# Optimization experiments

Measured on AMD Instinct MI355X. Metric: run time of the kernel, lower is better.

## Reference

```python
import jax, jax.numpy as jnp
import numpy as np

B, C_IN, T = 32, 22, 5000
EMB, P = 64, 100
HOP, NFFT, SR = 25, 128, 250
MIN_SZ, MAX_SZ = 10, 100
OC = 40
SCALES = (9, 25, 49)
FC = OC * len(SCALES)
_freqs = np.arange(NFFT // 2 + 1) * SR / NFFT
MU_IDX = np.nonzero((_freqs >= 8) & (_freqs <= 13))[0]   # bins 5,6
BETA_IDX = np.nonzero((_freqs >= 13) & (_freqs <= 30))[0]  # bins 7..15


def setup_inputs() -> dict:
    key = jax.random.key(0)
    k = iter(jax.random.split(key, 16))
    inp = {"x": jax.random.normal(next(k), (B, C_IN, T), jnp.float32)}
    for i, s in enumerate(SCALES):
        inp[f"ms{i}_w1"] = jax.random.normal(next(k), (OC, 1, 1, s), jnp.float32) * 0.05
        inp[f"ms{i}_b1"] = jnp.zeros((OC,), jnp.float32)
        inp[f"ms{i}_w2"] = jax.random.normal(next(k), (OC, OC, C_IN, 1), jnp.float32) * 0.05
        inp[f"ms{i}_b2"] = jnp.zeros((OC,), jnp.float32)
        inp[f"ms{i}_g"] = jnp.ones((OC,), jnp.float32)
        inp[f"ms{i}_bt"] = jnp.zeros((OC,), jnp.float32)
        inp[f"ms{i}_m"] = jnp.zeros((OC,), jnp.float32)
        inp[f"ms{i}_v"] = jnp.ones((OC,), jnp.float32)
    inp["a_w1"] = jax.random.normal(next(k), (C_IN // 2, C_IN, 3), jnp.float32) * 0.05
    inp["a_b1"] = jnp.zeros((C_IN // 2,), jnp.float32)
    inp["a_g"] = jnp.ones((C_IN // 2,), jnp.float32)
    inp["a_bt"] = jnp.zeros((C_IN // 2,), jnp.float32)
    inp["a_m"] = jnp.zeros((C_IN // 2,), jnp.float32)
    inp["a_v"] = jnp.ones((C_IN // 2,), jnp.float32)
    inp["a_w2"] = jax.random.normal(next(k), (1, C_IN // 2, 1), jnp.float32) * 0.05
    inp["a_b2"] = jnp.zeros((1,), jnp.float32)
    inp["proj_w"] = jax.random.normal(next(k), (EMB, FC, 1), jnp.float32) * 0.05
    inp["proj_b"] = jnp.zeros((EMB,), jnp.float32)
    return inp


def _conv1d(x, w, pad):
    return jax.lax.conv_general_dilated(x, w, (1,), [(pad, pad)],
                                        dimension_numbers=("NCH", "OIH", "NCH"))


def _bn(y, g, bt, m, v):  # eval-mode BatchNorm over channel dim of [B, C, T]
    return (y - m[None, :, None]) * jax.lax.rsqrt(v[None, :, None] + 1e-5) * g[None, :, None] + bt[None, :, None]


def _branch(x, w1, b1, w2, b2, g, bt, m, v):
    # Conv2d(1,OC,(1,ks)) on [B,1,C,T] == per-channel 1D conv over time.
    oc, _, _, ks = w1.shape
    b_, c_, t_ = x.shape
    y = _conv1d(x.reshape(b_ * c_, 1, t_), w1.reshape(oc, 1, ks), (ks - 1) // 2) + b1[None, :, None]
    y = y.reshape(b_, c_, oc, t_).transpose(0, 2, 1, 3)            # [B, OC, C, T]
    # Conv2d(OC,OC,(C,1)) collapses the channel (height) dim.
    y = jnp.einsum("oih,biht->bot", w2[..., 0], y) + b2[None, :, None]
    return jax.nn.elu(_bn(y, g, bt, m, v))                         # [B, OC, T]


def _stft_power(x):
    # torchaudio Spectrogram: center=True, reflect pad, periodic hann, power=2
    pad = NFFT // 2
    xp = jnp.pad(x, ((0, 0), (0, 0), (pad, pad)), mode="reflect")
    nfr = T // HOP  # module truncates to t // hop frames
    idx = jnp.arange(nfr)[:, None] * HOP + jnp.arange(NFFT)[None, :]
    win = 0.5 * (1.0 - jnp.cos(2.0 * jnp.pi * jnp.arange(NFFT) / NFFT))
    frames = xp[..., idx] * win                                    # [B, C, nfr, NFFT]
    spec = jnp.fft.rfft(frames, axis=-1)
    return spec.real ** 2 + spec.imag ** 2                         # [B, C, nfr, NFFT//2+1]


def _interp_linear(a, n):  # F.interpolate(mode='linear', align_corners=False) on [B, L]
    L = a.shape[-1]
    pos = jnp.clip((jnp.arange(n) + 0.5) * (L / n) - 0.5, 0.0, L - 1.0)
    lo = jnp.floor(pos).astype(jnp.int32)
    hi = jnp.minimum(lo + 1, L - 1)
    w = pos - lo
    return a[:, lo] * (1.0 - w) + a[:, hi] * w


def _adaptive_grid(act):
    w = 1.0 / (act + 1e-6)
    w = w / jnp.sum(w, axis=1, keepdims=True)
    gs = jnp.clip(w * T, MIN_SZ, MAX_SZ)
    gs = gs * (T / jnp.sum(gs, axis=1, keepdims=True))
    gsr = jnp.round(gs).astype(jnp.int32)
    gsr = gsr.at[:, -1].add(T - jnp.sum(gsr, axis=1))
    gsf = jnp.clip(gsr, MIN_SZ, MAX_SZ)
    gsf = gsf.at[:, -1].add(T - jnp.sum(gsf, axis=1))
    return jnp.where(gsf < MIN_SZ, MIN_SZ, gsf)


def _forward(x, ms0_w1, ms0_b1, ms0_w2, ms0_b2, ms0_g, ms0_bt, ms0_m, ms0_v,
             ms1_w1, ms1_b1, ms1_w2, ms1_b2, ms1_g, ms1_bt, ms1_m, ms1_v,
             ms2_w1, ms2_b1, ms2_w2, ms2_b2, ms2_g, ms2_bt, ms2_m, ms2_v,
             a_w1, a_b1, a_g, a_bt, a_m, a_v, a_w2, a_b2, proj_w, proj_b):
    # ---- frequency-domain activity detector ----
    spec = _stft_power(x)                                          # [B, C, 200, F]
    comb = spec[..., MU_IDX].mean(-1) + spec[..., BETA_IDX].mean(-1)  # [B, C, 200]
    a = jax.nn.relu(_bn(_conv1d(comb, a_w1, 1) + a_b1[None, :, None], a_g, a_bt, a_m, a_v))
    a = jnp.einsum("oi,bit->bot", a_w2[..., 0], a)[:, 0] + a_b2[0]
    activity = jax.nn.sigmoid(a)                                   # [B, 200]
    act_i = _interp_linear(activity, P)                            # [B, P]
    grid = _adaptive_grid(act_i)                                   # [B, P] int32, sums ~= T
    ends = jnp.cumsum(grid, axis=1)
    starts = ends - grid
    # ---- multi-scale CNN features ----
    feats = jnp.concatenate([
        _branch(x, ms0_w1, ms0_b1, ms0_w2, ms0_b2, ms0_g, ms0_bt, ms0_m, ms0_v),
        _branch(x, ms1_w1, ms1_b1, ms1_w2, ms1_b2, ms1_g, ms1_bt, ms1_m, ms1_v),
        _branch(x, ms2_w1, ms2_b1, ms2_w2, ms2_b2, ms2_g, ms2_bt, ms2_m, ms2_v)],
        axis=1)                                                    # [B, FC, T]
    # ---- ragged per-patch avg+max pooling via segment reductions ----
    tix = jnp.arange(T)
    seg = jax.vmap(lambda e: jnp.searchsorted(e, tix, side="right"))(ends)  # [B,T] in [0,P]
    flat = (seg + jnp.arange(B)[:, None] * (P + 1)).reshape(-1)
    f = feats.transpose(0, 2, 1).reshape(B * T, FC)
    nseg = B * (P + 1)  # extra slot collects any overflow timesteps
    sums = jax.ops.segment_sum(f, flat, num_segments=nseg)
    cnt = jax.ops.segment_sum(jnp.ones((B * T, 1), f.dtype), flat, num_segments=nseg)
    mx = jax.ops.segment_max(f, flat, num_segments=nseg)
    avg = sums / jnp.maximum(cnt, 1.0)
    mx = jnp.where(cnt > 0, mx, 0.0)
    pooled = (avg + mx).reshape(B, P + 1, FC)[:, :P]               # combined avg+max
    valid = ((ends <= T) & (starts < ends))[..., None]
    pooled = jnp.where(valid, pooled, 0.0)
    emb = jnp.einsum("oc,bpc->bpo", proj_w[..., 0], pooled) + proj_b  # [B, P, EMB]
    return emb, grid, act_i


def reference(x, ms0_w1, ms0_b1, ms0_w2, ms0_b2, ms0_g, ms0_bt, ms0_m, ms0_v,
              ms1_w1, ms1_b1, ms1_w2, ms1_b2, ms1_g, ms1_bt, ms1_m, ms1_v,
              ms2_w1, ms2_b1, ms2_w2, ms2_b2, ms2_g, ms2_bt, ms2_m, ms2_v,
              a_w1, a_b1, a_g, a_bt, a_m, a_v, a_w2, a_b2, proj_w, proj_b):
    return _forward(x, ms0_w1, ms0_b1, ms0_w2, ms0_b2, ms0_g, ms0_bt, ms0_m, ms0_v,
                    ms1_w1, ms1_b1, ms1_w2, ms1_b2, ms1_g, ms1_bt, ms1_m, ms1_v,
                    ms2_w1, ms2_b1, ms2_w2, ms2_b2, ms2_g, ms2_bt, ms2_m, ms2_v,
                    a_w1, a_b1, a_g, a_bt, a_m, a_v, a_w2, a_b2, proj_w, proj_b)
```

## Files before the change

### kernel.cpp

```cpp
#include <hip/hip_runtime.h>
#include <hip/hip_bf16.h>
#include <hip/hip_fp8.h>
#include <math.h>
#include <string.h>

#define B 32
#define CIN 22
#define T 5000
#define EMB 64
#define P 100
#define HOP 25
#define OC 40
#define FC 120
#define NBIN 11
#define NFR 200

#define TCH 256
#define CROWS 304
#define RS8 40

#define XPAD 5128
#define TWROW 24

#define PLANE ((size_t)B * T * OC)

typedef __attribute__((ext_vector_type(4))) float f32x4;

__device__ __forceinline__ unsigned short f2bf(float f) {
  unsigned u = __float_as_uint(f);
  unsigned r = (u + 0x7FFFu + ((u >> 16) & 1u)) >> 16;
  return (unsigned short)r;
}
__device__ __forceinline__ float bf2f(unsigned short u) {
  return __uint_as_float(((unsigned)u) << 16);
}
__device__ __forceinline__ unsigned char f2fp8(float f) {
  __hip_fp8_e4m3 q(f);
  return (unsigned char)q.__x;
}
__device__ __forceinline__ float fast_elu(float y) {
  return y > 0.f ? y : (__builtin_amdgcn_exp2f(y * 1.44269504088896340736f) - 1.0f);
}
__device__ __forceinline__ unsigned pack2bf(float a, float b) {
  __hip_bfloat162 h = __float22bfloat162_rn(make_float2(a, b));
  unsigned u;
  memcpy(&u, &h, 4);
  return u;
}
__device__ __forceinline__ float wave_sum_f(float v) {
  #pragma unroll
  for (int off = 1; off < 64; off <<= 1) v += __shfl_xor(v, off);
  return v;
}
__device__ __forceinline__ int wave_sum_i(int v) {
  #pragma unroll
  for (int off = 1; off < 64; off <<= 1) v += __shfl_xor(v, off);
  return v;
}

struct SetupArgs {
  const float* w1[3]; const float* b1[3]; const float* w2[3]; const float* b2[3];
  const float* g[3];  const float* bt[3]; const float* m[3];  const float* v[3];
  unsigned char* pw8;
  float* A; float* Bc; float* tw;
};

__global__ __launch_bounds__(256) void setup_all(SetupArgs args) {
  int bx = blockIdx.x;
  int tid = threadIdx.x;
  if (bx < 63) {
    int id = bx * 256 + tid;
    if (id < 15936) {
      int fi = id >> 6;
      int lane = id & 63;
      int s, KS, fl;
      if (fi < 27)       { s = 0; KS = 9;  fl = fi; }
      else if (fi < 102) { s = 1; KS = 25; fl = fi - 27; }
      else               { s = 2; KS = 49; fl = fi - 102; }
      int k = fl / 3, ot = fl - k * 3;
      int m = lane & 15, hb = (lane >> 4) << 3;
      int o = ot * 16 + m;
      float val[8];
      #pragma unroll
      for (int j = 0; j < 8; ++j) val[j] = 0.f;
      if (o < OC && hb < CIN) {
        const float* w1 = args.w1[s];
        const float* w2 = args.w2[s];
        if (hb + 8 <= CIN) {
          for (int i = 0; i < OC; ++i) {
            float wv = w1[i * KS + k];
            const float* w2r = w2 + (size_t)(o * OC + i) * CIN + hb;
            float2 a0 = *(const float2*)(w2r + 0);
            float2 a1 = *(const float2*)(w2r + 2);
            float2 a2 = *(const float2*)(w2r + 4);
            float2 a3 = *(const float2*)(w2r + 6);
            val[0] = fmaf(a0.x, wv, val[0]); val[1] = fmaf(a0.y, wv, val[1]);
            val[2] = fmaf(a1.x, wv, val[2]); val[3] = fmaf(a1.y, wv, val[3]);
            val[4] = fmaf(a2.x, wv, val[4]); val[5] = fmaf(a2.y, wv, val[5]);
            val[6] = fmaf(a3.x, wv, val[6]); val[7] = fmaf(a3.y, wv, val[7]);
          }
        } else {
          for (int i = 0; i < OC; ++i) {
            float wv = w1[i * KS + k];
            const float* w2r = w2 + (size_t)(o * OC + i) * CIN + hb;
            float2 a0 = *(const float2*)(w2r + 0);
            float2 a1 = *(const float2*)(w2r + 2);
            float2 a2 = *(const float2*)(w2r + 4);
            val[0] = fmaf(a0.x, wv, val[0]); val[1] = fmaf(a0.y, wv, val[1]);
            val[2] = fmaf(a1.x, wv, val[2]); val[3] = fmaf(a1.y, wv, val[3]);
            val[4] = fmaf(a2.x, wv, val[4]); val[5] = fmaf(a2.y, wv, val[5]);
          }
        }
      }
      unsigned char bytes[8];
      #pragma unroll
      for (int j = 0; j < 8; ++j) bytes[j] = f2fp8(val[j]);
      long long pk;
      memcpy(&pk, bytes, 8);
      *(long long*)(args.pw8 + (size_t)fi * 512 + lane * 8) = pk;
    }
  } else if (bx < 69) {
    int id = (bx - 63) * 256 + tid;
    if (id < 1408) {
      int n = id & 127, k = id >> 7;
      const double PI = 3.14159265358979323846;
      double ang = -2.0 * PI * (double)((k + 5) * n) / 128.0;
      double win = 0.5 * (1.0 - cos(2.0 * PI * (double)n / 128.0));
      args.tw[n * TWROW + 2 * k]     = (float)(cos(ang) * win);
      args.tw[n * TWROW + 2 * k + 1] = (float)(sin(ang) * win);
    } else if (id < 1536) {
      int n = id - 1408;
      args.tw[n * TWROW + 22] = 0.f;
      args.tw[n * TWROW + 23] = 0.f;
    }
  } else {
    if (tid < 120) {
      int s = tid / 40, o = tid - s * 40;
      const float* w2 = args.w2[s];
      float sc = args.g[s][o] / sqrtf(args.v[s][o] + 1e-5f);
      float cc = args.b2[s][o];
      for (int i = 0; i < OC; ++i) {
        float sh = 0.f;
        for (int h = 0; h < CIN; ++h) sh += w2[(o * OC + i) * CIN + h];
        cc = fmaf(args.b1[s][i], sh, cc);
      }
      args.A[tid] = sc;
      args.Bc[tid] = cc * sc + (args.bt[s][o] - args.m[s][o] * sc);
    }
  }
}

__global__ __launch_bounds__(256) void stft_comb(const float* __restrict__ x,
                                                 const float* __restrict__ tw,
                                                 float* __restrict__ comb) {
  __shared__ float xsh[XPAD];
  int bc = blockIdx.x;
  const float* xr = x + (size_t)bc * T;
  int tid = threadIdx.x;
  for (int i = tid; i < XPAD; i += 256) {
    int mm = i - 64;
    mm = (mm < 0) ? -mm : mm;
    mm = (mm >= T) ? (2 * T - 2 - mm) : mm;
    xsh[i] = xr[mm];
  }
  __syncthreads();
  int fr = tid;
  if (fr < NFR) {
    float cr[NBIN], ci[NBIN];
    #pragma unroll
    for (int k = 0; k < NBIN; ++k) { cr[k] = 0.f; ci[k] = 0.f; }
    const float* xw = xsh + fr * HOP;
    #pragma unroll 2
    for (int n = 0; n < 128; ++n) {
      float xv = xw[n];
      const float4* t4 = reinterpret_cast<const float4*>(tw + n * TWROW);
      float4 w0 = t4[0], w1 = t4[1], w2 = t4[2], w3 = t4[3], w4 = t4[4], w5 = t4[5];
      cr[0] = fmaf(xv, w0.x, cr[0]); ci[0] = fmaf(xv, w0.y, ci[0]);
      cr[1] = fmaf(xv, w0.z, cr[1]); ci[1] = fmaf(xv, w0.w, ci[1]);
      cr[2] = fmaf(xv, w1.x, cr[2]); ci[2] = fmaf(xv, w1.y, ci[2]);
      cr[3] = fmaf(xv, w1.z, cr[3]); ci[3] = fmaf(xv, w1.w, ci[3]);
      cr[4] = fmaf(xv, w2.x, cr[4]); ci[4] = fmaf(xv, w2.y, ci[4]);
      cr[5] = fmaf(xv, w2.z, cr[5]); ci[5] = fmaf(xv, w2.w, ci[5]);
      cr[6] = fmaf(xv, w3.x, cr[6]); ci[6] = fmaf(xv, w3.y, ci[6]);
      cr[7] = fmaf(xv, w3.z, cr[7]); ci[7] = fmaf(xv, w3.w, ci[7]);
      cr[8] = fmaf(xv, w4.x, cr[8]); ci[8] = fmaf(xv, w4.y, ci[8]);
      cr[9] = fmaf(xv, w4.z, cr[9]); ci[9] = fmaf(xv, w4.w, ci[9]);
      cr[10] = fmaf(xv, w5.x, cr[10]); ci[10] = fmaf(xv, w5.y, ci[10]);
    }
    float p[NBIN];
    #pragma unroll
    for (int k = 0; k < NBIN; ++k) p[k] = cr[k] * cr[k] + ci[k] * ci[k];
    float beta = 0.f;
    #pragma unroll
    for (int k = 2; k < NBIN; ++k) beta += p[k];
    comb[bc * NFR + fr] = 0.5f * (p[0] + p[1]) + beta * (1.f / 9.f);
  }
}

struct MidSmem {
  union {
    struct {
      float cl[CIN * NFR];
      float actL[NFR];
      float aiL[P];
      float fL[P];
      int giL[P];
      int sI[P];
      float red;
    } a;
    unsigned char xs8[CROWS * RS8];
  };
};

template <int KS, int FB, int SBASE>
__device__ __forceinline__ void scale_body(const unsigned char* __restrict__ xs8,
                                           const unsigned char* __restrict__ pw8,
                                           const float* __restrict__ Aff,
                                           const float* __restrict__ Bff,
                                           unsigned short* __restrict__ fplane,
                                           int b, int t0, int wt0, int lane) {
  constexpr int PAD = (KS - 1) / 2;
  const int n = lane & 15, q = lane >> 4;
  f32x4 acc[3][4];
  #pragma unroll
  for (int ot = 0; ot < 3; ++ot)
    #pragma unroll
    for (int ti = 0; ti < 4; ++ti)
      acc[ot][ti] = (f32x4){0.f, 0.f, 0.f, 0.f};

  const unsigned char* pws = pw8 + (size_t)FB * 512 + lane * 8;
  const unsigned char* xrow = xs8 + (24 - PAD + wt0 + n) * RS8 + q * 8;
  long long A0 = *(const long long*)(pws);
  long long A1 = *(const long long*)(pws + 512);
  long long A2 = *(const long long*)(pws + 1024);
  long long B0 = *(const long long*)(xrow);
  long long B1 = *(const long long*)(xrow + 16 * RS8);
  long long B2 = *(const long long*)(xrow + 32 * RS8);
  long long B3 = *(const long long*)(xrow + 48 * RS8);
  #pragma unroll 2
  for (int k = 0; k < KS - 1; ++k) {
    const unsigned char* p = pws + (size_t)(k + 1) * 1536;
    long long nA0 = *(const long long*)(p);
    long long nA1 = *(const long long*)(p + 512);
    long long nA2 = *(const long long*)(p + 1024);
    const unsigned char* xr = xrow + (k + 1) * RS8;
    long long nB0 = *(const long long*)(xr);
    long long nB1 = *(const long long*)(xr + 16 * RS8);
    long long nB2 = *(const long long*)(xr + 32 * RS8);
    long long nB3 = *(const long long*)(xr + 48 * RS8);
    acc[0][0] = __builtin_amdgcn_mfma_f32_16x16x32_fp8_fp8(A0, B0, acc[0][0], 0, 0, 0);
    acc[1][0] = __builtin_amdgcn_mfma_f32_16x16x32_fp8_fp8(A1, B0, acc[1][0], 0, 0, 0);
    acc[2][0] = __builtin_amdgcn_mfma_f32_16x16x32_fp8_fp8(A2, B0, acc[2][0], 0, 0, 0);
    acc[0][1] = __builtin_amdgcn_mfma_f32_16x16x32_fp8_fp8(A0, B1, acc[0][1], 0, 0, 0);
    acc[1][1] = __builtin_amdgcn_mfma_f32_16x16x32_fp8_fp8(A1, B1, acc[1][1], 0, 0, 0);
    acc[2][1] = __builtin_amdgcn_mfma_f32_16x16x32_fp8_fp8(A2, B1, acc[2][1], 0, 0, 0);
    acc[0][2] = __builtin_amdgcn_mfma_f32_16x16x32_fp8_fp8(A0, B2, acc[0][2], 0, 0, 0);
    acc[1][2] = __builtin_amdgcn_mfma_f32_16x16x32_fp8_fp8(A1, B2, acc[1][2], 0, 0, 0);
    acc[2][2] = __builtin_amdgcn_mfma_f32_16x16x32_fp8_fp8(A2, B2, acc[2][2], 0, 0, 0);
    acc[0][3] = __builtin_amdgcn_mfma_f32_16x16x32_fp8_fp8(A0, B3, acc[0][3], 0, 0, 0);
    acc[1][3] = __builtin_amdgcn_mfma_f32_16x16x32_fp8_fp8(A1, B3, acc[1][3], 0, 0, 0);
    acc[2][3] = __builtin_amdgcn_mfma_f32_16x16x32_fp8_fp8(A2, B3, acc[2][3], 0, 0, 0);
    A0 = nA0; A1 = nA1; A2 = nA2;
    B0 = nB0; B1 = nB1; B2 = nB2; B3 = nB3;
  }
  acc[0][0] = __builtin_amdgcn_mfma_f32_16x16x32_fp8_fp8(A0, B0, acc[0][0], 0, 0, 0);
  acc[1][0] = __builtin_amdgcn_mfma_f32_16x16x32_fp8_fp8(A1, B0, acc[1][0], 0, 0, 0);
  acc[2][0] = __builtin_amdgcn_mfma_f32_16x16x32_fp8_fp8(A2, B0, acc[2][0], 0, 0, 0);
  acc[0][1] = __builtin_amdgcn_mfma_f32_16x16x32_fp8_fp8(A0, B1, acc[0][1], 0, 0, 0);
  acc[1][1] = __builtin_amdgcn_mfma_f32_16x16x32_fp8_fp8(A1, B1, acc[1][1], 0, 0, 0);
  acc[2][1] = __builtin_amdgcn_mfma_f32_16x16x32_fp8_fp8(A2, B1, acc[2][1], 0, 0, 0);
  acc[0][2] = __builtin_amdgcn_mfma_f32_16x16x32_fp8_fp8(A0, B2, acc[0][2], 0, 0, 0);
  acc[1][2] = __builtin_amdgcn_mfma_f32_16x16x32_fp8_fp8(A1, B2, acc[1][2], 0, 0, 0);
  acc[2][2] = __builtin_amdgcn_mfma_f32_16x16x32_fp8_fp8(A2, B2, acc[2][2], 0, 0, 0);
  acc[0][3] = __builtin_amdgcn_mfma_f32_16x16x32_fp8_fp8(A0, B3, acc[0][3], 0, 0, 0);
  acc[1][3] = __builtin_amdgcn_mfma_f32_16x16x32_fp8_fp8(A1, B3, acc[1][3], 0, 0, 0);
  acc[2][3] = __builtin_amdgcn_mfma_f32_16x16x32_fp8_fp8(A2, B3, acc[2][3], 0, 0, 0);

  #pragma unroll
  for (int ot = 0; ot < 3; ++ot) {
    int obase = ot * 16 + q * 4;
    if (obase < OC) {
      float Av0 = Aff[SBASE + obase + 0], Bv0 = Bff[SBASE + obase + 0];
      float Av1 = Aff[SBASE + obase + 1], Bv1 = Bff[SBASE + obase + 1];
      float Av2 = Aff[SBASE + obase + 2], Bv2 = Bff[SBASE + obase + 2];
      float Av3 = Aff[SBASE + obase + 3], Bv3 = Bff[SBASE + obase + 3];
      #pragma unroll
      for (int ti = 0; ti < 4; ++ti) {
        int tt = t0 + wt0 + ti * 16 + n;
        if (tt < T) {
          uint2 pk;
          pk.x = pack2bf(fast_elu(fmaf(acc[ot][ti][0], Av0, Bv0)),
                         fast_elu(fmaf(acc[ot][ti][1], Av1, Bv1)));
          pk.y = pack2bf(fast_elu(fmaf(acc[ot][ti][2], Av2, Bv2)),
                         fast_elu(fmaf(acc[ot][ti][3], Av3, Bv3)));
          *reinterpret_cast<uint2*>(fplane + (size_t)(b * T + tt) * OC + obase) = pk;
        }
      }
    }
  }
}

struct MidArgs {
  const float* x;
  const unsigned char* pw8;
  const float* Aff; const float* Bff;
  unsigned short* feats;
  const float* comb;
  const float* aw1; const float* ab1;
  const float* ag;  const float* abt;
  const float* am;  const float* av;
  const float* aw2; const float* ab2;
  float* out_grid; float* out_acti;
  int* ends_i; int* grid_i;
};

__global__ __launch_bounds__(256) void mid_all(MidArgs args) {
  __shared__ MidSmem sm;
  int bx = blockIdx.x;
  int tid = threadIdx.x;
  if (bx >= B) {
    int cx = bx - B;
    int b = cx / 20, t0 = (cx - b * 20) * TCH;
    for (int i = tid; i < CROWS * RS8 / 4; i += 256)
      reinterpret_cast<unsigned*>(sm.xs8)[i] = 0u;
    __syncthreads();
    for (int idx = tid; idx < CIN * CROWS; idx += 256) {
      int h = idx / CROWS, tl = idx - h * CROWS;
      int gt = t0 - 24 + tl;
      float v = (gt >= 0 && gt < T) ? args.x[(size_t)(b * CIN + h) * T + gt] : 0.f;
      sm.xs8[tl * RS8 + h] = f2fp8(v);
    }
    __syncthreads();
    int wv = tid >> 6, lane = tid & 63;
    int wt0 = wv * 64;
    scale_body<9, 0, 0>(sm.xs8, args.pw8, args.Aff, args.Bff, args.feats, b, t0, wt0, lane);
    scale_body<25, 27, 40>(sm.xs8, args.pw8, args.Aff, args.Bff, args.feats + PLANE, b, t0, wt0, lane);
    scale_body<49, 102, 80>(sm.xs8, args.pw8, args.Aff, args.Bff, args.feats + 2 * PLANE, b, t0, wt0, lane);
  } else {
    int b = bx;
    for (int i = tid; i < CIN * NFR; i += 256) sm.a.cl[i] = args.comb[b * CIN * NFR + i];
    __syncthreads();
    int t = tid;
    if (t < NFR) {
      float z = args.ab2[0];
      for (int o = 0; o < 11; ++o) {
        float s = args.ab1[o];
        for (int i = 0; i < CIN; ++i) {
          const float* wr = args.aw1 + o * 66 + i * 3;
          const float* crow = sm.a.cl + i * NFR;
          if (t > 0)       s = fmaf(wr[0], crow[t - 1], s);
          s = fmaf(wr[1], crow[t], s);
          if (t < NFR - 1) s = fmaf(wr[2], crow[t + 1], s);
        }
        float rs = 1.0f / sqrtf(args.av[o] + 1e-5f);
        float y = (s - args.am[o]) * rs * args.ag[o] + args.abt[o];
        y = fmaxf(y, 0.f);
        z = fmaf(args.aw2[o], y, z);
      }
      sm.a.actL[t] = 1.f / (1.f + expf(-z));
    }
    __syncthreads();
    if (t < P) {
      float ai = 0.5f * (sm.a.actL[2 * t] + sm.a.actL[2 * t + 1]);
      sm.a.aiL[t] = ai;
      args.out_acti[b * P + t] = ai;
      sm.a.fL[t] = 1.f / (ai + 1e-6f);
    }
    __syncthreads();
    if (t < 64) {
      float v = sm.a.fL[t] + ((t + 64 < P) ? sm.a.fL[t + 64] : 0.f);
      v = wave_sum_f(v);
      if (t == 0) sm.a.red = v;
    }
    __syncthreads();
    float sw = sm.a.red;
    if (t < P) {
      float ggv = (sm.a.fL[t] / sw) * 5000.f;
      ggv = fminf(fmaxf(ggv, 10.f), 100.f);
      sm.a.fL[t] = ggv;
    }
    __syncthreads();
    if (t < 64) {
      float v = sm.a.fL[t] + ((t + 64 < P) ? sm.a.fL[t + 64] : 0.f);
      v = wave_sum_f(v);
      if (t == 0) sm.a.red = v;
    }
    __syncthreads();
    float r = 5000.f / sm.a.red;
    if (t < P) sm.a.giL[t] = (int)rintf(sm.a.fL[t] * r);
    __syncthreads();
    if (t < 64) {
      int v = sm.a.giL[t] + ((t + 64 < P) ? sm.a.giL[t + 64] : 0);
      v = wave_sum_i(v);
      if (t == 0) sm.a.red = __int_as_float(v);
    }
    __syncthreads();
    if (t == P - 1) sm.a.giL[P - 1] += 5000 - __float_as_int(sm.a.red);
    __syncthreads();
    if (t < P) sm.a.giL[t] = min(max(sm.a.giL[t], 10), 100);
    __syncthreads();
    if (t < 64) {
      int v = sm.a.giL[t] + ((t + 64 < P) ? sm.a.giL[t + 64] : 0);
      v = wave_sum_i(v);
      if (t == 0) sm.a.red = __int_as_float(v);
    }
    __syncthreads();
    if (t == P - 1) sm.a.giL[P - 1] += 5000 - __float_as_int(sm.a.red);
    __syncthreads();
    if (t < P) sm.a.sI[t] = max(sm.a.giL[t], 10);
    __syncthreads();
    #pragma unroll
    for (int off = 1; off < P; off <<= 1) {
      int v = 0;
      if (t < P && t >= off) v = sm.a.sI[t - off];
      __syncthreads();
      if (t < P) sm.a.sI[t] += v;
      __syncthreads();
    }
    if (t < P) {
      int g2 = max(sm.a.giL[t], 10);
      args.out_grid[b * P + t] = (float)g2;
      args.grid_i[b * P + t] = g2;
      args.ends_i[b * P + t] = sm.a.sI[t];
    }
  }
}

__global__ __launch_bounds__(256) void pool_proj(const unsigned short* __restrict__ feats,
                                                 const int* __restrict__ ends_i,
                                                 const int* __restrict__ grid_i,
                                                 const float* __restrict__ proj_w,
                                                 const float* __restrict__ proj_b,
                                                 float* __restrict__ out_emb) {
  int bp = blockIdx.x;
  int b = bp / P;
  int end = ends_i[bp];
  int gr = grid_i[bp];
  int start = end - gr;
  __shared__ float lds_s[16 * FC];
  __shared__ float lds_m[16 * FC];
  __shared__ float pooled[FC];
  int tid = threadIdx.x;
  bool valid = (end <= T);
  int g = tid % 15;
  int r = tid / 15;
  if (valid && r < 16) {
    float s[8], m[8];
    #pragma unroll
    for (int j = 0; j < 8; ++j) { s[j] = 0.f; m[j] = -INFINITY; }
    int pl = g / 5, g2 = g - pl * 5;
    const unsigned short* base = feats + (size_t)pl * PLANE + (size_t)(b * T + start) * OC + g2 * 8;
    for (int i = r; i < gr; i += 16) {
      uint4 u4 = *reinterpret_cast<const uint4*>(base + (size_t)i * OC);
      unsigned w[4] = {u4.x, u4.y, u4.z, u4.w};
      #pragma unroll
      for (int j = 0; j < 4; ++j) {
        float v0 = bf2f((unsigned short)(w[j] & 0xffffu));
        float v1 = bf2f((unsigned short)(w[j] >> 16));
        s[2 * j] += v0; s[2 * j + 1] += v1;
        m[2 * j] = fmaxf(m[2 * j], v0); m[2 * j + 1] = fmaxf(m[2 * j + 1], v1);
      }
    }
    #pragma unroll
    for (int j = 0; j < 8; ++j) {
      lds_s[r * FC + g * 8 + j] = s[j];
      lds_m[r * FC + g * 8 + j] = m[j];
    }
  }
  __syncthreads();
  if (tid < FC) {
    if (valid) {
      float s = 0.f, mx = -INFINITY;
      #pragma unroll
      for (int rr = 0; rr < 16; ++rr) {
        s += lds_s[rr * FC + tid];
        mx = fmaxf(mx, lds_m[rr * FC + tid]);
      }
      pooled[tid] = s / (float)gr + mx;
    } else {
      pooled[tid] = 0.f;
    }
  }
  __syncthreads();
  if (tid < EMB) {
    float e = proj_b[tid];
    const float* wr = proj_w + tid * FC;
    #pragma unroll 8
    for (int c = 0; c < FC; ++c) e = fmaf(wr[c], pooled[c], e);
    out_emb[(size_t)bp * EMB + tid] = e;
  }
}

extern "C" void kernel_launch(void* const* d_in, const int* in_sizes, int n_in,
                              void* d_out, int out_size, void* d_ws, size_t ws_size,
                              hipStream_t stream) {
  const float* x = (const float*)d_in[0];
  const float* aw1 = (const float*)d_in[25];
  const float* ab1 = (const float*)d_in[26];
  const float* ag  = (const float*)d_in[27];
  const float* abt = (const float*)d_in[28];
  const float* am  = (const float*)d_in[29];
  const float* av  = (const float*)d_in[30];
  const float* aw2 = (const float*)d_in[31];
  const float* ab2 = (const float*)d_in[32];
  const float* proj_w = (const float*)d_in[33];
  const float* proj_b = (const float*)d_in[34];

  float* wsf = (float*)d_ws;
  float* A    = wsf;
  float* Bc   = wsf + 120;
  float* tw   = wsf + 240;
  float* comb = wsf + 4096;
  int* ends_i = (int*)(wsf + 144896);
  int* grid_i = (int*)(wsf + 148096);
  unsigned char* pw8 = (unsigned char*)(wsf + 151296);
  unsigned short* feats = (unsigned short*)(wsf + 215040);

  float* out      = (float*)d_out;
  float* out_emb  = out;
  float* out_grid = out + 204800;
  float* out_acti = out + 208000;

  SetupArgs sa;
  MidArgs ma;
  for (int s = 0; s < 3; ++s) {
    sa.w1[s] = (const float*)d_in[1 + 8 * s];
    sa.b1[s] = (const float*)d_in[2 + 8 * s];
    sa.w2[s] = (const float*)d_in[3 + 8 * s];
    sa.b2[s] = (const float*)d_in[4 + 8 * s];
    sa.g[s]  = (const float*)d_in[5 + 8 * s];
    sa.bt[s] = (const float*)d_in[6 + 8 * s];
    sa.m[s]  = (const float*)d_in[7 + 8 * s];
    sa.v[s]  = (const float*)d_in[8 + 8 * s];
  }
  sa.pw8 = pw8; sa.A = A; sa.Bc = Bc; sa.tw = tw;

  ma.x = x; ma.pw8 = pw8; ma.Aff = A; ma.Bff = Bc; ma.feats = feats;
  ma.comb = comb; ma.aw1 = aw1; ma.ab1 = ab1; ma.ag = ag; ma.abt = abt;
  ma.am = am; ma.av = av; ma.aw2 = aw2; ma.ab2 = ab2;
  ma.out_grid = out_grid; ma.out_acti = out_acti;
  ma.ends_i = ends_i; ma.grid_i = grid_i;

  setup_all<<<70, 256, 0, stream>>>(sa);
  stft_comb<<<B * CIN, 256, 0, stream>>>(x, tw, comb);
  mid_all<<<B + 20 * B, 256, 0, stream>>>(ma);
  pool_proj<<<B * P, 256, 0, stream>>>(feats, ends_i, grid_i, proj_w, proj_b, out_emb);
}
```

Measured before the change: 256.6 us.

## Fuse STFT with multiscale conv kernel and split activation/grid into own kernel

The STFT band-power blocks now share a launch with the FP8 MFMA multiscale convolution blocks, and the activation/grid computation moves into a small separate kernel that runs afterwards. This lets the independent STFT and convolution work run concurrently instead of serially, so the conv no longer waits on the STFT kernel. It also raises wave priority around the MFMA loop with s_setprio. The trade-offs are an extra small kernel launch and a union of shared memory whose size is set by the larger STFT buffer.

Measured after the change: 287.7 us. +12.1%, slower.

```diff
diff --git a/kernel.cpp b/kernel.cpp
--- a/kernel.cpp
+++ b/kernel.cpp
@@ -18,6 +18,7 @@
 #define TCH 256
 #define CROWS 304
 #define RS8 40
+#define NCONV (20 * B)
 
 #define XPAD 5128
 #define TWROW 24
@@ -150,64 +151,9 @@
   }
 }
 
-__global__ __launch_bounds__(256) void stft_comb(const float* __restrict__ x,
-                                                 const float* __restrict__ tw,
-                                                 float* __restrict__ comb) {
-  __shared__ float xsh[XPAD];
-  int bc = blockIdx.x;
-  const float* xr = x + (size_t)bc * T;
-  int tid = threadIdx.x;
-  for (int i = tid; i < XPAD; i += 256) {
-    int mm = i - 64;
-    mm = (mm < 0) ? -mm : mm;
-    mm = (mm >= T) ? (2 * T - 2 - mm) : mm;
-    xsh[i] = xr[mm];
-  }
-  __syncthreads();
-  int fr = tid;
-  if (fr < NFR) {
-    float cr[NBIN], ci[NBIN];
-    #pragma unroll
-    for (int k = 0; k < NBIN; ++k) { cr[k] = 0.f; ci[k] = 0.f; }
-    const float* xw = xsh + fr * HOP;
-    #pragma unroll 2
-    for (int n = 0; n < 128; ++n) {
-      float xv = xw[n];
-      const float4* t4 = reinterpret_cast<const float4*>(tw + n * TWROW);
-      float4 w0 = t4[0], w1 = t4[1], w2 = t4[2], w3 = t4[3], w4 = t4[4], w5 = t4[5];
-      cr[0] = fmaf(xv, w0.x, cr[0]); ci[0] = fmaf(xv, w0.y, ci[0]);
-      cr[1] = fmaf(xv, w0.z, cr[1]); ci[1] = fmaf(xv, w0.w, ci[1]);
-      cr[2] = fmaf(xv, w1.x, cr[2]); ci[2] = fmaf(xv, w1.y, ci[2]);
-      cr[3] = fmaf(xv, w1.z, cr[3]); ci[3] = fmaf(xv, w1.w, ci[3]);
-      cr[4] = fmaf(xv, w2.x, cr[4]); ci[4] = fmaf(xv, w2.y, ci[4]);
-      cr[5] = fmaf(xv, w2.z, cr[5]); ci[5] = fmaf(xv, w2.w, ci[5]);
-      cr[6] = fmaf(xv, w3.x, cr[6]); ci[6] = fmaf(xv, w3.y, ci[6]);
-      cr[7] = fmaf(xv, w3.z, cr[7]); ci[7] = fmaf(xv, w3.w, ci[7]);
-      cr[8] = fmaf(xv, w4.x, cr[8]); ci[8] = fmaf(xv, w4.y, ci[8]);
-      cr[9] = fmaf(xv, w4.z, cr[9]); ci[9] = fmaf(xv, w4.w, ci[9]);
-      cr[10] = fmaf(xv, w5.x, cr[10]); ci[10] = fmaf(xv, w5.y, ci[10]);
-    }
-    float p[NBIN];
-    #pragma unroll
-    for (int k = 0; k < NBIN; ++k) p[k] = cr[k] * cr[k] + ci[k] * ci[k];
-    float beta = 0.f;
-    #pragma unroll
-    for (int k = 2; k < NBIN; ++k) beta += p[k];
-    comb[bc * NFR + fr] = 0.5f * (p[0] + p[1]) + beta * (1.f / 9.f);
-  }
-}
-
-struct MidSmem {
+struct SCSmem {
   union {
-    struct {
-      float cl[CIN * NFR];
-      float actL[NFR];
-      float aiL[P];
-      float fL[P];
-      int giL[P];
-      int sI[P];
-      float red;
-    } a;
+    float xsh[XPAD];
     unsigned char xs8[CROWS * RS8];
   };
 };
@@ -230,6 +176,7 @@
 
   const unsigned char* pws = pw8 + (size_t)FB * 512 + lane * 8;
   const unsigned char* xrow = xs8 + (24 - PAD + wt0 + n) * RS8 + q * 8;
+  __builtin_amdgcn_s_setprio(1);
   long long A0 = *(const long long*)(pws);
   long long A1 = *(const long long*)(pws + 512);
   long long A2 = *(const long long*)(pws + 1024);
@@ -275,6 +222,7 @@
   acc[0][3] = __builtin_amdgcn_mfma_f32_16x16x32_fp8_fp8(A0, B3, acc[0][3], 0, 0, 0);
   acc[1][3] = __builtin_amdgcn_mfma_f32_16x16x32_fp8_fp8(A1, B3, acc[1][3], 0, 0, 0);
   acc[2][3] = __builtin_amdgcn_mfma_f32_16x16x32_fp8_fp8(A2, B3, acc[2][3], 0, 0, 0);
+  __builtin_amdgcn_s_setprio(0);
 
   #pragma unroll
   for (int ot = 0; ot < 3; ++ot) {
@@ -300,11 +248,92 @@
   }
 }
 
-struct MidArgs {
+struct SCArgs {
   const float* x;
   const unsigned char* pw8;
   const float* Aff; const float* Bff;
   unsigned short* feats;
+  const float* tw;
+  float* comb;
+};
+
+__global__ __launch_bounds__(256) void stft_conv(SCArgs args) {
+  __shared__ SCSmem sm;
+  int bx = blockIdx.x;
+  int tid = threadIdx.x;
+  if (bx < NCONV) {
+    int b = bx / 20, t0 = (bx - b * 20) * TCH;
+    for (int i = tid; i < CROWS * RS8 / 4; i += 256)
+      reinterpret_cast<unsigned*>(sm.xs8)[i] = 0u;
+    __syncthreads();
+    for (int idx = tid; idx < CIN * CROWS; idx += 256) {
+      int h = idx / CROWS, tl = idx - h * CROWS;
+      int gt = t0 - 24 + tl;
+      float v = (gt >= 0 && gt < T) ? args.x[(size_t)(b * CIN + h) * T + gt] : 0.f;
+      sm.xs8[tl * RS8 + h] = f2fp8(v);
+    }
+    __syncthreads();
+    int wv = tid >> 6, lane = tid & 63;
+    int wt0 = wv * 64;
+    scale_body<9, 0, 0>(sm.xs8, args.pw8, args.Aff, args.Bff, args.feats, b, t0, wt0, lane);
+    scale_body<25, 27, 40>(sm.xs8, args.pw8, args.Aff, args.Bff, args.feats + PLANE, b, t0, wt0, lane);
+    scale_body<49, 102, 80>(sm.xs8, args.pw8, args.Aff, args.Bff, args.feats + 2 * PLANE, b, t0, wt0, lane);
+  } else {
+    int bc = bx - NCONV;
+    const float* xr = args.x + (size_t)bc * T;
+    for (int i = tid; i < XPAD; i += 256) {
+      int mm = i - 64;
+      mm = (mm < 0) ? -mm : mm;
+      mm = (mm >= T) ? (2 * T - 2 - mm) : mm;
+      sm.xsh[i] = xr[mm];
+    }
+    __syncthreads();
+    int fr = tid;
+    if (fr < NFR) {
+      float cr[NBIN], ci[NBIN];
+      #pragma unroll
+      for (int k = 0; k < NBIN; ++k) { cr[k] = 0.f; ci[k] = 0.f; }
+      const float* xw = sm.xsh + fr * HOP;
+      const float* tw = args.tw;
+      #pragma unroll 2
+      for (int n = 0; n < 128; ++n) {
+        float xv = xw[n];
+        const float4* t4 = reinterpret_cast<const float4*>(tw + n * TWROW);
+        float4 w0 = t4[0], w1 = t4[1], w2 = t4[2], w3 = t4[3], w4 = t4[4], w5 = t4[5];
+        cr[0] = fmaf(xv, w0.x, cr[0]); ci[0] = fmaf(xv, w0.y, ci[0]);
+        cr[1] = fmaf(xv, w0.z, cr[1]); ci[1] = fmaf(xv, w0.w, ci[1]);
+        cr[2] = fmaf(xv, w1.x, cr[2]); ci[2] = fmaf(xv, w1.y, ci[2]);
+        cr[3] = fmaf(xv, w1.z, cr[3]); ci[3] = fmaf(xv, w1.w, ci[3]);
+        cr[4] = fmaf(xv, w2.x, cr[4]); ci[4] = fmaf(xv, w2.y, ci[4]);
+        cr[5] = fmaf(xv, w2.z, cr[5]); ci[5] = fmaf(xv, w2.w, ci[5]);
+        cr[6] = fmaf(xv, w3.x, cr[6]); ci[6] = fmaf(xv, w3.y, ci[6]);
+        cr[7] = fmaf(xv, w3.z, cr[7]); ci[7] = fmaf(xv, w3.w, ci[7]);
+        cr[8] = fmaf(xv, w4.x, cr[8]); ci[8] = fmaf(xv, w4.y, ci[8]);
+        cr[9] = fmaf(xv, w4.z, cr[9]); ci[9] = fmaf(xv, w4.w, ci[9]);
+        cr[10] = fmaf(xv, w5.x, cr[10]); ci[10] = fmaf(xv, w5.y, ci[10]);
+      }
+      float p[NBIN];
+      #pragma unroll
+      for (int k = 0; k < NBIN; ++k) p[k] = cr[k] * cr[k] + ci[k] * ci[k];
+      float beta = 0.f;
+      #pragma unroll
+      for (int k = 2; k < NBIN; ++k) beta += p[k];
+      args.comb[bc * NFR + fr] = 0.5f * (p[0] + p[1]) + beta * (1.f / 9.f);
+    }
+  }
+}
+
+struct ActSmem {
+  float cl[CIN * NFR];
+  float actL[NFR];
+  float aiL[P];
+  float fL[P];
+  int giL[P];
+  int sI[P];
+  float red;
+};
+
+struct ActArgs {
   const float* comb;
   const float* aw1; const float* ab1;
   const float* ag;  const float* abt;
@@ -314,115 +343,94 @@
   int* ends_i; int* grid_i;
 };
 
-__global__ __launch_bounds__(256) void mid_all(MidArgs args) {
-  __shared__ MidSmem sm;
-  int bx = blockIdx.x;
+__global__ __launch_bounds__(256) void act_grid(ActArgs args) {
+  __shared__ ActSmem sm;
+  int b = blockIdx.x;
   int tid = threadIdx.x;
-  if (bx >= B) {
-    int cx = bx - B;
-    int b = cx / 20, t0 = (cx - b * 20) * TCH;
-    for (int i = tid; i < CROWS * RS8 / 4; i += 256)
-      reinterpret_cast<unsigned*>(sm.xs8)[i] = 0u;
+  for (int i = tid; i < CIN * NFR; i += 256) sm.cl[i] = args.comb[b * CIN * NFR + i];
+  __syncthreads();
+  int t = tid;
+  if (t < NFR) {
+    float z = args.ab2[0];
+    for (int o = 0; o < 11; ++o) {
+      float s = args.ab1[o];
+      for (int i = 0; i < CIN; ++i) {
+        const float* wr = args.aw1 + o * 66 + i * 3;
+        const float* crow = sm.cl + i * NFR;
+        if (t > 0)       s = fmaf(wr[0], crow[t - 1], s);
+        s = fmaf(wr[1], crow[t], s);
+        if (t < NFR - 1) s = fmaf(wr[2], crow[t + 1], s);
+      }
+      float rs = 1.0f / sqrtf(args.av[o] + 1e-5f);
+      float y = (s - args.am[o]) * rs * args.ag[o] + args.abt[o];
+      y = fmaxf(y, 0.f);
+      z = fmaf(args.aw2[o], y, z);
+    }
+    sm.actL[t] = 1.f / (1.f + expf(-z));
+  }
+  __syncthreads();
+  if (t < P) {
+    float ai = 0.5f * (sm.actL[2 * t] + sm.actL[2 * t + 1]);
+    sm.aiL[t] = ai;
+    args.out_acti[b * P + t] = ai;
+    sm.fL[t] = 1.f / (ai + 1e-6f);
+  }
+  __syncthreads();
+  if (t < 64) {
+    float v = sm.fL[t] + ((t + 64 < P) ? sm.fL[t + 64] : 0.f);
+    v = wave_sum_f(v);
+    if (t == 0) sm.red = v;
+  }
+  __syncthreads();
+  float sw = sm.red;
+  if (t < P) {
+    float ggv = (sm.fL[t] / sw) * 5000.f;
+    ggv = fminf(fmaxf(ggv, 10.f), 100.f);
+    sm.fL[t] = ggv;
+  }
+  __syncthreads();
+  if (t < 64) {
+    float v = sm.fL[t] + ((t + 64 < P) ? sm.fL[t + 64] : 0.f);
+    v = wave_sum_f(v);
+    if (t == 0) sm.red = v;
+  }
+  __syncthreads();
+  float r = 5000.f / sm.red;
+  if (t < P) sm.giL[t] = (int)rintf(sm.fL[t] * r);
+  __syncthreads();
+  if (t < 64) {
+    int v = sm.giL[t] + ((t + 64 < P) ? sm.giL[t + 64] : 0);
+    v = wave_sum_i(v);
+    if (t == 0) sm.red = __int_as_float(v);
+  }
+  __syncthreads();
+  if (t == P - 1) sm.giL[P - 1] += 5000 - __float_as_int(sm.red);
+  __syncthreads();
+  if (t < P) sm.giL[t] = min(max(sm.giL[t], 10), 100);
+  __syncthreads();
+  if (t < 64) {
+    int v = sm.giL[t] + ((t + 64 < P) ? sm.giL[t + 64] : 0);
+    v = wave_sum_i(v);
+    if (t == 0) sm.red = __int_as_float(v);
+  }
+  __syncthreads();
+  if (t == P - 1) sm.giL[P - 1] += 5000 - __float_as_int(sm.red);
+  __syncthreads();
+  if (t < P) sm.sI[t] = max(sm.giL[t], 10);
+  __syncthreads();
+  #pragma unroll
+  for (int off = 1; off < P; off <<= 1) {
+    int v = 0;
+    if (t < P && t >= off) v = sm.sI[t - off];
     __syncthreads();
-    for (int idx = tid; idx < CIN * CROWS; idx += 256) {
-      int h = idx / CROWS, tl = idx - h * CROWS;
-      int gt = t0 - 24 + tl;
-      float v = (gt >= 0 && gt < T) ? args.x[(size_t)(b * CIN + h) * T + gt] : 0.f;
-      sm.xs8[tl * RS8 + h] = f2fp8(v);
-    }
+    if (t < P) sm.sI[t] += v;
     __syncthreads();
-    int wv = tid >> 6, lane = tid & 63;
-    int wt0 = wv * 64;
-    scale_body<9, 0, 0>(sm.xs8, args.pw8, args.Aff, args.Bff, args.feats, b, t0, wt0, lane);
-    scale_body<25, 27, 40>(sm.xs8, args.pw8, args.Aff, args.Bff, args.feats + PLANE, b, t0, wt0, lane);
-    scale_body<49, 102, 80>(sm.xs8, args.pw8, args.Aff, args.Bff, args.feats + 2 * PLANE, b, t0, wt0, lane);
-  } else {
-    int b = bx;
-    for (int i = tid; i < CIN * NFR; i += 256) sm.a.cl[i] = args.comb[b * CIN * NFR + i];
-    __syncthreads();
-    int t = tid;
-    if (t < NFR) {
-      float z = args.ab2[0];
-      for (int o = 0; o < 11; ++o) {
-        float s = args.ab1[o];
-        for (int i = 0; i < CIN; ++i) {
-          const float* wr = args.aw1 + o * 66 + i * 3;
-          const float* crow = sm.a.cl + i * NFR;
-          if (t > 0)       s = fmaf(wr[0], crow[t - 1], s);
-          s = fmaf(wr[1], crow[t], s);
-          if (t < NFR - 1) s = fmaf(wr[2], crow[t + 1], s);
-        }
-        float rs = 1.0f / sqrtf(args.av[o] + 1e-5f);
-        float y = (s - args.am[o]) * rs * args.ag[o] + args.abt[o];
-        y = fmaxf(y, 0.f);
-        z = fmaf(args.aw2[o], y, z);
-      }
-      sm.a.actL[t] = 1.f / (1.f + expf(-z));
-    }
-    __syncthreads();
-    if (t < P) {
-      float ai = 0.5f * (sm.a.actL[2 * t] + sm.a.actL[2 * t + 1]);
-      sm.a.aiL[t] = ai;
-      args.out_acti[b * P + t] = ai;
-      sm.a.fL[t] = 1.f / (ai + 1e-6f);
-    }
-    __syncthreads();
-    if (t < 64) {
-      float v = sm.a.fL[t] + ((t + 64 < P) ? sm.a.fL[t + 64] : 0.f);
-      v = wave_sum_f(v);
-      if (t == 0) sm.a.red = v;
-    }
-    __syncthreads();
-    float sw = sm.a.red;
-    if (t < P) {
-      float ggv = (sm.a.fL[t] / sw) * 5000.f;
-      ggv = fminf(fmaxf(ggv, 10.f), 100.f);
-      sm.a.fL[t] = ggv;
-    }
-    __syncthreads();
-    if (t < 64) {
-      float v = sm.a.fL[t] + ((t + 64 < P) ? sm.a.fL[t + 64] : 0.f);
-      v = wave_sum_f(v);
-      if (t == 0) sm.a.red = v;
-    }
-    __syncthreads();
-    float r = 5000.f / sm.a.red;
-    if (t < P) sm.a.giL[t] = (int)rintf(sm.a.fL[t] * r);
-    __syncthreads();
-    if (t < 64) {
-      int v = sm.a.giL[t] + ((t + 64 < P) ? sm.a.giL[t + 64] : 0);
-      v = wave_sum_i(v);
-      if (t == 0) sm.a.red = __int_as_float(v);
-    }
-    __syncthreads();
-    if (t == P - 1) sm.a.giL[P - 1] += 5000 - __float_as_int(sm.a.red);
-    __syncthreads();
-    if (t < P) sm.a.giL[t] = min(max(sm.a.giL[t], 10), 100);
-    __syncthreads();
-    if (t < 64) {
-      int v = sm.a.giL[t] + ((t + 64 < P) ? sm.a.giL[t + 64] : 0);
-      v = wave_sum_i(v);
-      if (t == 0) sm.a.red = __int_as_float(v);
-    }
-    __syncthreads();
-    if (t == P - 1) sm.a.giL[P - 1] += 5000 - __float_as_int(sm.a.red);
-    __syncthreads();
-    if (t < P) sm.a.sI[t] = max(sm.a.giL[t], 10);
-    __syncthreads();
-    #pragma unroll
-    for (int off = 1; off < P; off <<= 1) {
-      int v = 0;
-      if (t < P && t >= off) v = sm.a.sI[t - off];
-      __syncthreads();
-      if (t < P) sm.a.sI[t] += v;
-      __syncthreads();
-    }
-    if (t < P) {
-      int g2 = max(sm.a.giL[t], 10);
-      args.out_grid[b * P + t] = (float)g2;
-      args.grid_i[b * P + t] = g2;
-      args.ends_i[b * P + t] = sm.a.sI[t];
-    }
+  }
+  if (t < P) {
+    int g2 = max(sm.giL[t], 10);
+    args.out_grid[b * P + t] = (float)g2;
+    args.grid_i[b * P + t] = g2;
+    args.ends_i[b * P + t] = sm.sI[t];
   }
 }
 
@@ -522,7 +530,6 @@
   float* out_acti = out + 208000;
 
   SetupArgs sa;
-  MidArgs ma;
   for (int s = 0; s < 3; ++s) {
     sa.w1[s] = (const float*)d_in[1 + 8 * s];
     sa.b1[s] = (const float*)d_in[2 + 8 * s];
@@ -535,14 +542,18 @@
   }
   sa.pw8 = pw8; sa.A = A; sa.Bc = Bc; sa.tw = tw;
 
-  ma.x = x; ma.pw8 = pw8; ma.Aff = A; ma.Bff = Bc; ma.feats = feats;
-  ma.comb = comb; ma.aw1 = aw1; ma.ab1 = ab1; ma.ag = ag; ma.abt = abt;
-  ma.am = am; ma.av = av; ma.aw2 = aw2; ma.ab2 = ab2;
-  ma.out_grid = out_grid; ma.out_acti = out_acti;
-  ma.ends_i = ends_i; ma.grid_i = grid_i;
+  SCArgs sc;
+  sc.x = x; sc.pw8 = pw8; sc.Aff = A; sc.Bff = Bc; sc.feats = feats;
+  sc.tw = tw; sc.comb = comb;
+
+  ActArgs aa;
+  aa.comb = comb; aa.aw1 = aw1; aa.ab1 = ab1; aa.ag = ag; aa.abt = abt;
+  aa.am = am; aa.av = av; aa.aw2 = aw2; aa.ab2 = ab2;
+  aa.out_grid = out_grid; aa.out_acti = out_acti;
+  aa.ends_i = ends_i; aa.grid_i = grid_i;
 
   setup_all<<<70, 256, 0, stream>>>(sa);
-  stft_comb<<<B * CIN, 256, 0, stream>>>(x, tw, comb);
-  mid_all<<<B + 20 * B, 256, 0, stream>>>(ma);
+  stft_conv<<<NCONV + B * CIN, 256, 0, stream>>>(sc);
+  act_grid<<<B, 256, 0, stream>>>(aa);
   pool_proj<<<B * P, 256, 0, stream>>>(feats, ends_i, grid_i, proj_w, proj_b, out_emb);
 }
```

## Pre-transpose x to padded fp8 rows in setup and DMA tiles into LDS

Applied to the files above, without the earlier changes.

Adds a pass in setup_all that converts x to fp8 once, transposed into time-major rows of 40 bytes with zero padding for halos. mid_all conv blocks then fill shared memory with global_load_lds direct copies (12 KB per block) instead of zeroing LDS and gathering and converting strided fp32 values per element. This removes the repeated overlapping conversion work and the uncoalesced channel-strided loads. In exchange it adds an extra global write and read of about 6.6 MB and more setup blocks. It also enlarges the shared union, and each block now copies 307 rows where it previously staged 304.

New measurement: 250.5 us, median of 2. 2.4% less time.

```diff
diff --git a/kernel.cpp b/kernel.cpp
--- a/kernel.cpp
+++ b/kernel.cpp
@@ -18,6 +18,7 @@
 #define TCH 256
 #define CROWS 304
 #define RS8 40
+#define XROWS 5184
 
 #define XPAD 5128
 #define TWROW 24
@@ -61,7 +62,9 @@
 struct SetupArgs {
   const float* w1[3]; const float* b1[3]; const float* w2[3]; const float* b2[3];
   const float* g[3];  const float* bt[3]; const float* m[3];  const float* v[3];
+  const float* x;
   unsigned char* pw8;
+  unsigned char* x8t;
   float* A; float* Bc; float* tw;
 };
 
@@ -133,7 +136,7 @@
       args.tw[n * TWROW + 22] = 0.f;
       args.tw[n * TWROW + 23] = 0.f;
     }
-  } else {
+  } else if (bx == 69) {
     if (tid < 120) {
       int s = tid / 40, o = tid - s * 40;
       const float* w2 = args.w2[s];
@@ -146,6 +149,28 @@
       }
       args.A[tid] = sc;
       args.Bc[tid] = cc * sc + (args.bt[s][o] - args.m[s][o] * sc);
+    }
+  } else {
+    int idx = (bx - 70) * 256 + tid;
+    if (idx < B * XROWS) {
+      int b = idx / XROWS;
+      int ridx = idx - b * XROWS;
+      int t = ridx - 24;
+      unsigned char row[RS8];
+      if (t >= 0 && t < T) {
+        const float* xb = args.x + (size_t)b * CIN * T + t;
+        #pragma unroll
+        for (int ch = 0; ch < CIN; ++ch) row[ch] = f2fp8(xb[(size_t)ch * T]);
+        #pragma unroll
+        for (int ch = CIN; ch < RS8; ++ch) row[ch] = 0;
+      } else {
+        #pragma unroll
+        for (int ch = 0; ch < RS8; ++ch) row[ch] = 0;
+      }
+      long long v[5];
+      memcpy(v, row, RS8);
+      long long* dst = (long long*)(args.x8t + (size_t)idx * RS8);
+      dst[0] = v[0]; dst[1] = v[1]; dst[2] = v[2]; dst[3] = v[3]; dst[4] = v[4];
     }
   }
 }
@@ -197,7 +222,7 @@
   }
 }
 
-struct MidSmem {
+struct __align__(16) MidSmem {
   union {
     struct {
       float cl[CIN * NFR];
@@ -208,7 +233,7 @@
       int sI[P];
       float red;
     } a;
-    unsigned char xs8[CROWS * RS8];
+    unsigned char xs8[12288];
   };
 };
 
@@ -301,7 +326,7 @@
 }
 
 struct MidArgs {
-  const float* x;
+  const unsigned char* x8t;
   const unsigned char* pw8;
   const float* Aff; const float* Bff;
   unsigned short* feats;
@@ -321,14 +346,16 @@
   if (bx >= B) {
     int cx = bx - B;
     int b = cx / 20, t0 = (cx - b * 20) * TCH;
-    for (int i = tid; i < CROWS * RS8 / 4; i += 256)
-      reinterpret_cast<unsigned*>(sm.xs8)[i] = 0u;
-    __syncthreads();
-    for (int idx = tid; idx < CIN * CROWS; idx += 256) {
-      int h = idx / CROWS, tl = idx - h * CROWS;
-      int gt = t0 - 24 + tl;
-      float v = (gt >= 0 && gt < T) ? args.x[(size_t)(b * CIN + h) * T + gt] : 0.f;
-      sm.xs8[tl * RS8 + h] = f2fp8(v);
+    {
+      int wv = tid >> 6, lane = tid & 63;
+      const unsigned char* gsrc = args.x8t + ((size_t)b * XROWS + t0) * RS8;
+      #pragma unroll
+      for (int c = 0; c < 3; ++c) {
+        int off = wv * 3072 + c * 1024;
+        __builtin_amdgcn_global_load_lds(
+            reinterpret_cast<const unsigned*>(gsrc + off + lane * 16),
+            reinterpret_cast<unsigned*>(sm.xs8 + off), 16, 0, 0);
+      }
     }
     __syncthreads();
     int wv = tid >> 6, lane = tid & 63;
@@ -515,6 +542,7 @@
   int* grid_i = (int*)(wsf + 148096);
   unsigned char* pw8 = (unsigned char*)(wsf + 151296);
   unsigned short* feats = (unsigned short*)(wsf + 215040);
+  unsigned char* x8t = (unsigned char*)(feats + 3 * PLANE);
 
   float* out      = (float*)d_out;
   float* out_emb  = out;
@@ -522,7 +550,6 @@
   float* out_acti = out + 208000;
 
   SetupArgs sa;
-  MidArgs ma;
   for (int s = 0; s < 3; ++s) {
     sa.w1[s] = (const float*)d_in[1 + 8 * s];
     sa.b1[s] = (const float*)d_in[2 + 8 * s];
@@ -533,15 +560,17 @@
     sa.m[s]  = (const float*)d_in[7 + 8 * s];
     sa.v[s]  = (const float*)d_in[8 + 8 * s];
   }
-  sa.pw8 = pw8; sa.A = A; sa.Bc = Bc; sa.tw = tw;
-
-  ma.x = x; ma.pw8 = pw8; ma.Aff = A; ma.Bff = Bc; ma.feats = feats;
+  sa.x = x; sa.pw8 = pw8; sa.x8t = x8t; sa.A = A; sa.Bc = Bc; sa.tw = tw;
+
+  MidArgs ma;
+  ma.x8t = x8t; ma.pw8 = pw8; ma.Aff = A; ma.Bff = Bc; ma.feats = feats;
   ma.comb = comb; ma.aw1 = aw1; ma.ab1 = ab1; ma.ag = ag; ma.abt = abt;
   ma.am = am; ma.av = av; ma.aw2 = aw2; ma.ab2 = ab2;
   ma.out_grid = out_grid; ma.out_acti = out_acti;
   ma.ends_i = ends_i; ma.grid_i = grid_i;
 
-  setup_all<<<70, 256, 0, stream>>>(sa);
+  int xblocks = (B * XROWS + 255) / 256;
+  setup_all<<<70 + xblocks, 256, 0, stream>>>(sa);
   stft_comb<<<B * CIN, 256, 0, stream>>>(x, tw, comb);
   mid_all<<<B + 20 * B, 256, 0, stream>>>(ma);
   pool_proj<<<B * P, 256, 0, stream>>>(feats, ends_i, grid_i, proj_w, proj_b, out_emb);
```
